# Kernel optimization log

Measured on AMD Instinct MI355X. Metric: run time of the kernel, lower is better.

Reference implementation:

```python
import jax, jax.numpy as jnp
import numpy as np

# dims (match init_kwargs)
L, D, H, K = 8, 384, 6, 64            # layers, hidden, rwkv heads, rwkv head dim
DI, MH, HD, DS, CK = 768, 12, 64, 64, 4  # mamba: d_inner, heads, head_dim, d_state, conv kernel
V, B, T = 32000, 1, 1024


def _rms(x, w, eps=1e-6):
    return w * x * jax.lax.rsqrt(jnp.mean(x * x, axis=-1, keepdims=True) + eps)


def _rwkv6(xn, Wr, Wk, Wv, Wg, Ww, w_bias, u, gn_w, gn_b, Wo):
    # RWKV6: data-dependent diagonal-decay linear attention
    Bb, Tt, Dd = xn.shape
    proj = lambda W: (xn @ W).reshape(Bb, Tt, H, K)
    r, k, v = proj(Wr), proj(Wk), proj(Wv)
    g = xn @ Wg                                        # [B,T,D]
    w = (xn @ Ww + w_bias).reshape(Bb, Tt, H, K)
    decay = jnp.exp(-jnp.exp(w))                       # in (0,1)

    def step(S, inp):                                  # S: [B,H,K,K] (key x value)
        r_t, k_t, v_t, d_t = inp                       # each [B,H,K]
        kv = k_t[..., :, None] * v_t[..., None, :]     # [B,H,K,K]
        o = jnp.einsum('bhk,bhkv->bhv', r_t, S + u[None, :, :, None] * kv)
        S = d_t[..., None] * S + kv
        return S, o

    tm = lambda a: jnp.moveaxis(a, 1, 0)               # time-major
    S0 = jnp.zeros((Bb, H, K, K), xn.dtype)
    _, o = jax.lax.scan(step, S0, (tm(r), tm(k), tm(v), tm(decay)))
    o = jnp.moveaxis(o, 0, 1)                          # [B,T,H,K]
    # per-head GroupNorm
    mu = jnp.mean(o, -1, keepdims=True)
    var = jnp.var(o, -1, keepdims=True)
    o = (o - mu) * jax.lax.rsqrt(var + 1e-5) * gn_w.reshape(H, K) + gn_b.reshape(H, K)
    o = o.reshape(Bb, Tt, Dd) * jax.nn.silu(g)
    return o @ Wo


def _mamba2(xn, W_in, conv_w, conv_b, dt_bias, A_log, Dp, mn_w, W_out):
    # Mamba2: selective scan with scalar A per head
    Bb, Tt, Dd = xn.shape
    zxbcdt = xn @ W_in                                 # [B,T, 2*DI + 2*DS + MH]
    z = zxbcdt[..., :DI]
    xBC = zxbcdt[..., DI:DI + DI + 2 * DS]
    dt = jax.nn.softplus(zxbcdt[..., -MH:] + dt_bias)  # [B,T,MH]
    # causal depthwise conv1d, kernel CK
    xp = jnp.pad(xBC, ((0, 0), (CK - 1, 0), (0, 0)))
    xBC = sum(xp[:, j:j + Tt, :] * conv_w[:, j] for j in range(CK)) + conv_b
    xBC = jax.nn.silu(xBC)
    xs = xBC[..., :DI].reshape(Bb, Tt, MH, HD)
    Bm = xBC[..., DI:DI + DS]                          # [B,T,DS]
    Cm = xBC[..., DI + DS:]                            # [B,T,DS]
    A = -jnp.exp(A_log)                                # [MH]

    def step(S, inp):                                  # S: [B,MH,HD,DS]
        x_t, B_t, C_t, dt_t = inp                      # [B,MH,HD],[B,DS],[B,DS],[B,MH]
        dA = jnp.exp(dt_t * A)                         # [B,MH]
        S = dA[..., None, None] * S + (dt_t[..., None] * x_t)[..., None] * B_t[:, None, None, :]
        y = jnp.einsum('bhps,bs->bhp', S, C_t) + Dp[None, :, None] * x_t
        return S, y

    tm = lambda a: jnp.moveaxis(a, 1, 0)
    S0 = jnp.zeros((Bb, MH, HD, DS), xn.dtype)
    _, y = jax.lax.scan(step, S0, (tm(xs), tm(Bm), tm(Cm), tm(dt)))
    y = jnp.moveaxis(y, 0, 1).reshape(Bb, Tt, DI)
    y = _rms(y * jax.nn.silu(z), mn_w)                 # gated RMSNorm
    return y @ W_out


def _forward(x, embed, ln_w, Wr, Wk, Wv, Wg, Ww, w_bias, u, gn_w, gn_b, Wo,
             W_in, conv_w, conv_b, dt_bias, A_log, Dp, mn_w, W_out,
             gw, gb, ffn_ln_w, ffn_w1, ffn_w2, ln_out_w):
    h = jnp.take(embed, x, axis=0)                     # [B,T,D]
    for i in range(L):
        xn = _rms(h, ln_w[i])
        o_r = _rwkv6(xn, Wr[i], Wk[i], Wv[i], Wg[i], Ww[i], w_bias[i], u[i], gn_w[i], gn_b[i], Wo[i])
        o_m = _mamba2(xn, W_in[i], conv_w[i], conv_b[i], dt_bias[i], A_log[i], Dp[i], mn_w[i], W_out[i])
        gate = jax.nn.sigmoid(jnp.concatenate([o_r, o_m], -1) @ gw[i] + gb[i])  # [B,T,1]
        h = h + gate * o_r + (1.0 - gate) * o_m
        hn = _rms(h, ffn_ln_w[i])
        h = h + jax.nn.gelu(hn @ ffn_w1[i], approximate=False) @ ffn_w2[i]
    h = _rms(h, ln_out_w)
    return h @ embed.T                                 # tied head -> [B,T,V]


def setup_inputs() -> dict:
    key = jax.random.key(0)
    ks = iter(jax.random.split(key, 32))
    n = lambda shape, s=0.02: jax.random.normal(next(ks), shape, jnp.float32) * s
    d = {}
    d['x'] = jax.random.randint(next(ks), (B, T), 0, V)
    d['embed'] = n((V, D))
    d['ln_w'] = jnp.ones((L, D), jnp.float32)
    d['Wr'] = n((L, D, D)); d['Wk'] = n((L, D, D)); d['Wv'] = n((L, D, D))
    d['Wg'] = n((L, D, D)); d['Ww'] = n((L, D, D))
    d['w_bias'] = n((L, D), 0.5)
    d['u'] = n((L, H, K), 0.5)
    d['gn_w'] = jnp.ones((L, D), jnp.float32)
    d['gn_b'] = jnp.zeros((L, D), jnp.float32)
    d['Wo'] = n((L, D, D))
    d['W_in'] = n((L, D, 2 * DI + 2 * DS + MH))
    d['conv_w'] = n((L, DI + 2 * DS, CK), 0.2)
    d['conv_b'] = jnp.zeros((L, DI + 2 * DS), jnp.float32)
    d['dt_bias'] = jax.random.uniform(next(ks), (L, MH), jnp.float32, -4.0, -1.0)
    d['A_log'] = jnp.log(jax.random.uniform(next(ks), (L, MH), jnp.float32, 1.0, 16.0))
    d['Dp'] = jnp.ones((L, MH), jnp.float32)
    d['mn_w'] = jnp.ones((L, DI), jnp.float32)
    d['W_out'] = n((L, DI, D))
    d['gw'] = n((L, 2 * D, 1), 0.01)
    d['gb'] = jnp.full((L, 1), float(np.log(0.3 / 0.7)), jnp.float32)
    d['ffn_ln_w'] = jnp.ones((L, D), jnp.float32)
    d['ffn_w1'] = n((L, D, 4 * D))
    d['ffn_w2'] = n((L, 4 * D, D))
    d['ln_out_w'] = jnp.ones((D,), jnp.float32)
    return d


def reference(x, embed, ln_w, Wr, Wk, Wv, Wg, Ww, w_bias, u, gn_w, gn_b, Wo,
              W_in, conv_w, conv_b, dt_bias, A_log, Dp, mn_w, W_out,
              gw, gb, ffn_ln_w, ffn_w1, ffn_w2, ln_out_w):
    return _forward(x, embed, ln_w, Wr, Wk, Wv, Wg, Ww, w_bias, u, gn_w, gn_b, Wo,
                    W_in, conv_w, conv_b, dt_bias, A_log, Dp, mn_w, W_out,
                    gw, gb, ffn_ln_w, ffn_w1, ffn_w2, ln_out_w)
```

## Files before the change

kernel.cpp:

```cpp
#include <hip/hip_runtime.h>
#include <math.h>

#define TT 1024
#define DD 384
#define NH 6
#define DI 768
#define MH 12
#define DS 64
#define NL 8
#define XDIM 1676
#define CONVC 896
#define NV 32000
#define PZS 3712
#define G_OFF 1152
#define W_OFF 1536
#define Z_OFF 1920
#define XBC_OFF 2688
#define DT_OFF 3584
#define CHK 32
#define NCH 32

typedef __attribute__((ext_vector_type(8))) short short8;
typedef __attribute__((ext_vector_type(4))) float f32x4;

__device__ __forceinline__ float siluf(float x) { return x / (1.f + expf(-x)); }
__device__ __forceinline__ float sigmoidf_(float x) { return 1.f / (1.f + expf(-x)); }
__device__ __forceinline__ float geluf(float x) {
  return 0.5f * x * (1.f + erff(x * 0.70710678118654752440f));
}
__device__ __forceinline__ unsigned short f2b(float x) {
  union { float f; unsigned int u; } v; v.f = x;
  unsigned int r = v.u + 0x7fffu + ((v.u >> 16) & 1u);
  return (unsigned short)(r >> 16);
}

#define GLDS(gp, lp) __builtin_amdgcn_global_load_lds( \
    (const __attribute__((address_space(1))) void*)(gp), \
    (__attribute__((address_space(3))) void*)(lp), 16, 0, 0)

template<int EPI>
__global__ __launch_bounds__(256) void gemm_bf16(
    const unsigned short* __restrict__ A, const unsigned short* __restrict__ Bt,
    float* __restrict__ C, unsigned short* __restrict__ Cb, int N, int K, int ldC)
{
  __shared__ unsigned short As[4096];
  __shared__ unsigned short Bs[4096];
  int tid = threadIdx.x;
  int wid = tid >> 6, lane = tid & 63;
  int m0 = blockIdx.y * 64, n0 = blockIdx.x * 64;
  int wr = wid >> 1, wc = wid & 1;
  int r0 = tid >> 3, ch = tid & 7;
  int scs = (ch ^ (r0 & 7)) * 8;
  const unsigned short* ga = A  + (size_t)(m0 + r0) * K + scs;
  const unsigned short* gb = Bt + (size_t)(n0 + r0) * K + scs;
  unsigned short* la = As + wid * 512;
  unsigned short* lb = Bs + wid * 512;
  int fr = lane & 15, fc = lane >> 4;
  f32x4 zz = {0.f, 0.f, 0.f, 0.f};
  f32x4 acc[2][2];
  acc[0][0] = zz; acc[0][1] = zz; acc[1][0] = zz; acc[1][1] = zz;

  int kper = K / (int)gridDim.z;
  int ks = blockIdx.z * kper, ke = ks + kper;
  size_t row32 = (size_t)32 * K;
  for (int k0 = ks; k0 < ke; k0 += 64) {
    GLDS(ga + k0, la);
    GLDS(ga + k0 + row32, la + 2048);
    GLDS(gb + k0, lb);
    GLDS(gb + k0 + row32, lb + 2048);
    __syncthreads();
#pragma unroll
    for (int kh = 0; kh < 2; ++kh) {
      short8 af[2], bf[2];
#pragma unroll
      for (int mg = 0; mg < 2; ++mg) {
        int ar = wr * 32 + mg * 16 + fr;
        af[mg] = *reinterpret_cast<const short8*>(&As[ar * 64 + (((kh * 4 + fc) ^ (ar & 7)) * 8)]);
      }
#pragma unroll
      for (int ng = 0; ng < 2; ++ng) {
        int br = wc * 32 + ng * 16 + fr;
        bf[ng] = *reinterpret_cast<const short8*>(&Bs[br * 64 + (((kh * 4 + fc) ^ (br & 7)) * 8)]);
      }
#pragma unroll
      for (int mg = 0; mg < 2; ++mg)
#pragma unroll
        for (int ng = 0; ng < 2; ++ng)
          acc[mg][ng] = __builtin_amdgcn_mfma_f32_16x16x32_bf16(af[mg], bf[ng], acc[mg][ng], 0, 0, 0);
    }
    __syncthreads();
  }
#pragma unroll
  for (int mg = 0; mg < 2; ++mg)
#pragma unroll
    for (int ng = 0; ng < 2; ++ng) {
      int col = n0 + wc * 32 + ng * 16 + fr;
      if (col < N) {
#pragma unroll
        for (int j = 0; j < 4; ++j) {
          int row = m0 + wr * 32 + mg * 16 + fc * 4 + j;
          if (EPI == 1)      Cb[(size_t)row * ldC + col] = f2b(geluf(acc[mg][ng][j]));
          else if (EPI == 3) atomicAdd(&C[(size_t)row * ldC + col], acc[mg][ng][j]);
          else               C[(size_t)row * ldC + col]  = acc[mg][ng][j];
        }
      }
    }
}

__global__ __launch_bounds__(256) void gemm_dual(
    const unsigned short* __restrict__ A0, const unsigned short* __restrict__ B0t,
    float* __restrict__ C0, int K0, int ld0, int nx0, int nb0,
    const unsigned short* __restrict__ A1, const unsigned short* __restrict__ B1t,
    float* __restrict__ C1, int K1, int ld1, int nx1)
{
  __shared__ unsigned short As[4096];
  __shared__ unsigned short Bs[4096];
  int b = blockIdx.x;
  const unsigned short *A, *Bt; float* C; int K, ldC, bx, by;
  if (b < nb0) { A = A0; Bt = B0t; C = C0; K = K0; ldC = ld0; bx = b % nx0; by = b / nx0; }
  else { b -= nb0; A = A1; Bt = B1t; C = C1; K = K1; ldC = ld1; bx = b % nx1; by = b / nx1; }
  int tid = threadIdx.x;
  int wid = tid >> 6, lane = tid & 63;
  int m0 = by * 64, n0 = bx * 64;
  int wr = wid >> 1, wc = wid & 1;
  int r0 = tid >> 3, ch = tid & 7;
  int scs = (ch ^ (r0 & 7)) * 8;
  const unsigned short* ga = A  + (size_t)(m0 + r0) * K + scs;
  const unsigned short* gb = Bt + (size_t)(n0 + r0) * K + scs;
  unsigned short* la = As + wid * 512;
  unsigned short* lb = Bs + wid * 512;
  int fr = lane & 15, fc = lane >> 4;
  f32x4 zz = {0.f, 0.f, 0.f, 0.f};
  f32x4 acc[2][2];
  acc[0][0] = zz; acc[0][1] = zz; acc[1][0] = zz; acc[1][1] = zz;
  size_t row32 = (size_t)32 * K;
  for (int k0 = 0; k0 < K; k0 += 64) {
    GLDS(ga + k0, la);
    GLDS(ga + k0 + row32, la + 2048);
    GLDS(gb + k0, lb);
    GLDS(gb + k0 + row32, lb + 2048);
    __syncthreads();
#pragma unroll
    for (int kh = 0; kh < 2; ++kh) {
      short8 af[2], bf[2];
// ... 8 lines not shown
        bf[ng] = *reinterpret_cast<const short8*>(&Bs[br * 64 + (((kh * 4 + fc) ^ (br & 7)) * 8)]);
      }
#pragma unroll
      for (int mg = 0; mg < 2; ++mg)
#pragma unroll
        for (int ng = 0; ng < 2; ++ng)
          acc[mg][ng] = __builtin_amdgcn_mfma_f32_16x16x32_bf16(af[mg], bf[ng], acc[mg][ng], 0, 0, 0);
    }
    __syncthreads();
  }
#pragma unroll
  for (int mg = 0; mg < 2; ++mg)
#pragma unroll
    for (int ng = 0; ng < 2; ++ng) {
      int col = n0 + wc * 32 + ng * 16 + fr;
#pragma unroll
      for (int j = 0; j < 4; ++j) {
        int row = m0 + wr * 32 + mg * 16 + fc * 4 + j;
        C[(size_t)row * ldC + col] = acc[mg][ng][j];
      }
    }
}

__global__ __launch_bounds__(256) void gemm128(
    const unsigned short* __restrict__ A, const unsigned short* __restrict__ Bt,
    float* __restrict__ C, int N, int K, int ldC)
{
  __shared__ unsigned short As[8192];
  __shared__ unsigned short Bs[8192];
  int tid = threadIdx.x;
  int wid = tid >> 6, lane = tid & 63;
  int m0 = blockIdx.y * 128, n0 = blockIdx.x * 128;
  int wr = wid >> 1, wc = wid & 1;
  int r0 = tid >> 3, ch = tid & 7;
  int scs = (ch ^ (r0 & 7)) * 8;
  const unsigned short* ga = A  + (size_t)(m0 + r0) * K + scs;
  const unsigned short* gb = Bt + (size_t)(n0 + r0) * K + scs;
  int fr = lane & 15, fc = lane >> 4;
  f32x4 zz = {0.f, 0.f, 0.f, 0.f};
  f32x4 acc[4][4];
#pragma unroll
  for (int i = 0; i < 4; i++)
#pragma unroll
    for (int j = 0; j < 4; j++) acc[i][j] = zz;

  size_t row32 = (size_t)32 * K;
  for (int k0 = 0; k0 < K; k0 += 64) {
#pragma unroll
    for (int i = 0; i < 4; ++i) {
      GLDS(ga + k0 + i * row32, As + i * 2048 + wid * 512);
      GLDS(gb + k0 + i * row32, Bs + i * 2048 + wid * 512);
    }
    __syncthreads();
#pragma unroll
    for (int kh = 0; kh < 2; ++kh) {
      short8 af[4], bf[4];
#pragma unroll
      for (int mg = 0; mg < 4; ++mg) {
        int ar = wr * 64 + mg * 16 + fr;
        af[mg] = *reinterpret_cast<const short8*>(&As[ar * 64 + (((kh * 4 + fc) ^ (ar & 7)) * 8)]);
      }
#pragma unroll
      for (int ng = 0; ng < 4; ++ng) {
        int br = wc * 64 + ng * 16 + fr;
        bf[ng] = *reinterpret_cast<const short8*>(&Bs[br * 64 + (((kh * 4 + fc) ^ (br & 7)) * 8)]);
      }
#pragma unroll
      for (int mg = 0; mg < 4; ++mg)
#pragma unroll
        for (int ng = 0; ng < 4; ++ng)
          acc[mg][ng] = __builtin_amdgcn_mfma_f32_16x16x32_bf16(af[mg], bf[ng], acc[mg][ng], 0, 0, 0);
    }
    __syncthreads();
  }
#pragma unroll
  for (int mg = 0; mg < 4; ++mg)
#pragma unroll
    for (int ng = 0; ng < 4; ++ng) {
      int col = n0 + wc * 64 + ng * 16 + fr;
      if (col < N) {
#pragma unroll
        for (int j = 0; j < 4; ++j) {
          int row = m0 + wr * 64 + mg * 16 + fc * 4 + j;
          C[(size_t)row * ldC + col] = acc[mg][ng][j];
        }
      }
    }
}

struct TCJob { const float* src; unsigned short* dst; int K, N, Npad, nx; size_t sStr, dStr; int tend; };
struct TC10 { TCJob j[10]; };

__global__ __launch_bounds__(256) void transconv_all(TC10 P)
{
  __shared__ float tile[32][33];
  int bid = blockIdx.x;
  int q = 0;
  while (bid >= P.j[q].tend) ++q;
  int tstart = (q == 0) ? 0 : P.j[q - 1].tend;
  TCJob jb = P.j[q];
  int local = bid - tstart;
  int bx = local % jb.nx, by = local / jb.nx;
  const float* src = jb.src + (size_t)blockIdx.y * jb.sStr;
  unsigned short* dst = jb.dst + (size_t)blockIdx.y * jb.dStr;
  int k0 = by * 32, n0 = bx * 32;
  int tx = threadIdx.x & 31, ty = threadIdx.x >> 5;
  for (int i = ty; i < 32; i += 8) {
    int k = k0 + i, n = n0 + tx;
    tile[i][tx] = (k < jb.K && n < jb.N) ? src[(size_t)k * jb.N + n] : 0.f;
  }
  __syncthreads();
  for (int i = ty; i < 32; i += 8) {
    int n = n0 + i, k = k0 + tx;
    if (n < jb.Npad && k < jb.K) dst[(size_t)n * jb.K + k] = f2b(tile[tx][i]);
  }
}

__global__ void conv_b16_kernel(const float* __restrict__ src, unsigned short* __restrict__ dst, int n)
{
  int idx = blockIdx.x * 256 + threadIdx.x;
  if (idx < n) dst[idx] = f2b(src[idx]);
}

__global__ void embed_kernel(const int* __restrict__ x, const float* __restrict__ embed,
                             float* __restrict__ h)
{
  int idx = blockIdx.x * 256 + threadIdx.x;
  if (idx < TT * DD) {
    int t = idx / DD, d = idx % DD;
    h[idx] = embed[(size_t)x[t] * DD + d];
  }
}

__global__ __launch_bounds__(256) void rms_kernel(const float* __restrict__ in,
                                                  const float* __restrict__ w,
                                                  unsigned short* __restrict__ out)
{
  int row = blockIdx.x * 4 + (threadIdx.x >> 6);
  int lane = threadIdx.x & 63;
  const float* r = in + (size_t)row * DD;
  float v[6]; float ss = 0.f;
#pragma unroll
  for (int j = 0; j < 6; ++j) { v[j] = r[lane + j * 64]; ss = fmaf(v[j], v[j], ss); }
#pragma unroll
  for (int s = 1; s < 64; s <<= 1) ss += __shfl_xor(ss, s);
  float scale = rsqrtf(ss * (1.f / DD) + 1e-6f);
#pragma unroll
  for (int j = 0; j < 6; ++j)
    out[(size_t)row * DD + lane + j * 64] = f2b(w[lane + j * 64] * v[j] * scale);
}

__global__ __launch_bounds__(256) void scanA_kernel(
    const float* __restrict__ PZ, const float* __restrict__ u, const float* __restrict__ wbias,
    float* __restrict__ so, float* __restrict__ rPb,
    float* __restrict__ MstR, float* __restrict__ DcR,
    const float* __restrict__ cw, const float* __restrict__ cbia,
    const float* __restrict__ dtbias,
    const float* __restrict__ Alog, const float* __restrict__ Dpw,
    float* __restrict__ yb, float* __restrict__ Ccb,
    float* __restrict__ MstM, float* __restrict__ DcM)
{
  __shared__ float smem[2 * 256 + 64];
  int b = blockIdx.x, tid = threadIdx.x;
  if (b < 192) {
    int h = b >> 5, c = b & 31;
    float* sbuf = smem; float* us = smem + 512;
    if (tid < 64) us[tid] = u[h * 64 + tid];
    int wv = tid >> 6, l = tid & 63;
    int vv = wv * 16 + (l & 15);
    int kc = l >> 4;
    int arr = tid >> 6, idx = tid & 63;
    int off = (arr == 0) ? 0 : (arr == 1) ? 384 : (arr == 2) ? W_OFF : 768;
// ... 215 lines not shown
    float4 s0 = sp[0], s1 = sp[1];
    ov[0] = s0.x + acc[0]; ov[1] = s0.y + acc[1]; ov[2] = s0.z + acc[2]; ov[3] = s0.w + acc[3];
    ov[4] = s1.x + acc[4]; ov[5] = s1.y + acc[5]; ov[6] = s1.z + acc[6]; ov[7] = s1.w + acc[7];
    float m_ = 0.f;
#pragma unroll
    for (int j = 0; j < 8; j++) m_ += ov[j];
    m_ += __shfl_xor(m_, 1); m_ += __shfl_xor(m_, 2); m_ += __shfl_xor(m_, 4);
    float mu = m_ * (1.f / 64.f);
    float vv = 0.f;
#pragma unroll
    for (int j = 0; j < 8; j++) { float d = ov[j] - mu; vv = fmaf(d, d, vv); }
    vv += __shfl_xor(vv, 1); vv += __shfl_xor(vv, 2); vv += __shfl_xor(vv, 4);
    float rstd = rsqrtf(vv * (1.f / 64.f) + 1e-5f);
#pragma unroll
    for (int j = 0; j < 8; j++) {
      int d = obase + q + j;
      float gv = PZ[(size_t)(t0 + t) * PZS + G_OFF + d];
      float o = fmaf((ov[j] - mu) * rstd, gnw[d], gnb[d]) * siluf(gv);
      gob[(size_t)(t0 + t) * DD + d] = f2b(o);
    }
  }
}

__global__ __launch_bounds__(256) void mamba_norm_kernel(const float* __restrict__ yb,
    const float* __restrict__ PZ, const float* __restrict__ mnw, unsigned short* __restrict__ out)
{
  int row = blockIdx.x * 4 + (threadIdx.x >> 6);
  int lane = threadIdx.x & 63;
  float v[12]; float ss = 0.f;
#pragma unroll
  for (int j = 0; j < 12; ++j) {
    int c = lane + j * 64;
    float z = PZ[(size_t)row * PZS + Z_OFF + c];
    float t = yb[(size_t)row * DI + c] * siluf(z);
    v[j] = t; ss = fmaf(t, t, ss);
  }
#pragma unroll
  for (int s = 1; s < 64; s <<= 1) ss += __shfl_xor(ss, s);
  float scale = rsqrtf(ss * (1.f / DI) + 1e-6f);
#pragma unroll
  for (int j = 0; j < 12; ++j) {
    int c = lane + j * 64;
    out[(size_t)row * DI + c] = f2b(v[j] * scale * mnw[c]);
  }
}

__global__ __launch_bounds__(256) void gate_rms_kernel(const float* __restrict__ orb,
    const float* __restrict__ omb, const float* __restrict__ gw,
    const float* __restrict__ gb, const float* __restrict__ flnw,
    float* __restrict__ h, unsigned short* __restrict__ xnb)
{
  int row = blockIdx.x * 4 + (threadIdx.x >> 6);
  int lane = threadIdx.x & 63;
  float a[6], bq[6]; float ss = 0.f;
#pragma unroll
  for (int j = 0; j < 6; ++j) {
    int c = lane + j * 64;
    a[j] = orb[(size_t)row * DD + c]; bq[j] = omb[(size_t)row * DD + c];
    ss += a[j] * gw[c] + bq[j] * gw[DD + c];
  }
#pragma unroll
  for (int s = 1; s < 64; s <<= 1) ss += __shfl_xor(ss, s);
  float gate = sigmoidf_(ss + gb[0]);
  float hn[6]; float ss2 = 0.f;
#pragma unroll
  for (int j = 0; j < 6; ++j) {
    int c = lane + j * 64;
    size_t ix = (size_t)row * DD + c;
    hn[j] = h[ix] + gate * a[j] + (1.f - gate) * bq[j];
    h[ix] = hn[j];
    ss2 = fmaf(hn[j], hn[j], ss2);
  }
#pragma unroll
  for (int s = 1; s < 64; s <<= 1) ss2 += __shfl_xor(ss2, s);
  float scale = rsqrtf(ss2 * (1.f / DD) + 1e-6f);
#pragma unroll
  for (int j = 0; j < 6; ++j) {
    int c = lane + j * 64;
    xnb[(size_t)row * DD + c] = f2b(flnw[c] * hn[j] * scale);
  }
}

extern "C" void kernel_launch(void* const* d_in, const int* in_sizes, int n_in,
                              void* d_out, int out_size, void* d_ws, size_t ws_size,
                              hipStream_t stream)
{
  const int*   x        = (const int*)  d_in[0];
  const float* embed    = (const float*)d_in[1];
  const float* ln_w     = (const float*)d_in[2];
  const float* Wr       = (const float*)d_in[3];
  const float* Wk       = (const float*)d_in[4];
  const float* Wv       = (const float*)d_in[5];
  const float* Wg       = (const float*)d_in[6];
  const float* Ww       = (const float*)d_in[7];
  const float* w_bias   = (const float*)d_in[8];
  const float* u        = (const float*)d_in[9];
  const float* gn_w     = (const float*)d_in[10];
  const float* gn_b     = (const float*)d_in[11];
  const float* Wo       = (const float*)d_in[12];
  const float* W_in     = (const float*)d_in[13];
  const float* conv_w   = (const float*)d_in[14];
  const float* conv_b   = (const float*)d_in[15];
  const float* dt_bias  = (const float*)d_in[16];
  const float* A_log    = (const float*)d_in[17];
  const float* Dp       = (const float*)d_in[18];
  const float* mn_w     = (const float*)d_in[19];
  const float* W_out    = (const float*)d_in[20];
  const float* gw       = (const float*)d_in[21];
  const float* gb       = (const float*)d_in[22];
  const float* ffn_ln_w = (const float*)d_in[23];
  const float* ffn_w1   = (const float*)d_in[24];
  const float* ffn_w2   = (const float*)d_in[25];
  const float* ln_out_w = (const float*)d_in[26];

  char* base = (char*)d_ws;
  size_t off = 0;
  auto alloc = [&](size_t bytes) { off = (off + 255) & ~(size_t)255; void* p = base + off; off += bytes; return p; };

  float* h    = (float*)alloc((size_t)TT * DD * 4);
  float* PZ   = (float*)alloc((size_t)TT * PZS * 4);
  float* yb   = (float*)alloc((size_t)TT * DI * 4);
  float* so   = (float*)alloc((size_t)TT * DD * 4);
  float* orb  = (float*)alloc((size_t)TT * DD * 4);
  float* omb  = (float*)alloc((size_t)TT * DD * 4);
  float* rPb  = (float*)alloc((size_t)TT * DD * 4);
  float* Ccb  = (float*)alloc((size_t)TT * DI * 4);
  float* MstR = (float*)alloc((size_t)NH * NCH * 4096 * 4);
  float* DcR  = (float*)alloc((size_t)NH * NCH * 64 * 4);
  float* MstM = (float*)alloc((size_t)MH * NCH * 4096 * 4);
  float* DcM  = (float*)alloc((size_t)MH * NCH * 4);
  unsigned short* xnb = (unsigned short*)alloc((size_t)TT * DD * 2);
  unsigned short* gob = (unsigned short*)alloc((size_t)TT * DD * 2);
  unsigned short* ynb = (unsigned short*)alloc((size_t)TT * DI * 2);
  unsigned short* fhb = (unsigned short*)alloc((size_t)TT * 1536 * 2);
  unsigned short* WallT = (unsigned short*)alloc((size_t)NL * PZS * 384 * 2);
  unsigned short* WoT   = (unsigned short*)alloc((size_t)NL * 384 * 384 * 2);
  unsigned short* WoutT = (unsigned short*)alloc((size_t)NL * 384 * 768 * 2);
  unsigned short* F1T   = (unsigned short*)alloc((size_t)NL * 1536 * 384 * 2);
  unsigned short* F2T   = (unsigned short*)alloc((size_t)NL * 384 * 1536 * 2);
  unsigned short* embB  = (unsigned short*)alloc((size_t)NV * DD * 2);
  (void)ws_size; (void)in_sizes; (void)n_in; (void)out_size;

  dim3 blk(256);
  int gTD = (TT * DD + 255) / 256;

  TC10 tc;
  int te = 0;
  auto setjob = [&](int q, const float* src, unsigned short* dst, int K, int N, int Npad,
                    int nx, int ny, size_t sStr, size_t dStr) {
    te += nx * ny;
    tc.j[q] = TCJob{src, dst, K, N, Npad, nx, sStr, dStr, te};
  };
  setjob(0, Wr, WallT + (size_t)0 * 384 * 384, 384, 384, 384, 12, 12, (size_t)384 * 384, (size_t)PZS * 384);
  setjob(1, Wk, WallT + (size_t)1 * 384 * 384, 384, 384, 384, 12, 12, (size_t)384 * 384, (size_t)PZS * 384);
  setjob(2, Wv, WallT + (size_t)2 * 384 * 384, 384, 384, 384, 12, 12, (size_t)384 * 384, (size_t)PZS * 384);
  setjob(3, Wg, WallT + (size_t)3 * 384 * 384, 384, 384, 384, 12, 12, (size_t)384 * 384, (size_t)PZS * 384);
  setjob(4, Ww, WallT + (size_t)4 * 384 * 384, 384, 384, 384, 12, 12, (size_t)384 * 384, (size_t)PZS * 384);
  setjob(5, W_in, WallT + (size_t)1920 * 384, 384, XDIM, 1792, 56, 12, (size_t)384 * XDIM, (size_t)PZS * 384);
  setjob(6, Wo, WoT, 384, 384, 384, 12, 12, (size_t)384 * 384, (size_t)384 * 384);
  setjob(7, W_out, WoutT, 768, 384, 384, 12, 24, (size_t)768 * 384, (size_t)384 * 768);
  setjob(8, ffn_w1, F1T, 384, 1536, 1536, 48, 12, (size_t)384 * 1536, (size_t)1536 * 384);
  setjob(9, ffn_w2, F2T, 1536, 384, 384, 12, 48, (size_t)1536 * 384, (size_t)384 * 1536);
  transconv_all<<<dim3(te, 8), blk, 0, stream>>>(tc);
  conv_b16_kernel<<<(NV * DD + 255) / 256, blk, 0, stream>>>(embed, embB, NV * DD);
  embed_kernel<<<gTD, blk, 0, stream>>>(x, embed, h);

  for (int i = 0; i < NL; ++i) {
    rms_kernel<<<256, blk, 0, stream>>>(h, ln_w + (size_t)i * DD, xnb);

    gemm_bf16<0><<<dim3(58, 16), blk, 0, stream>>>(
        xnb, WallT + (size_t)i * PZS * 384, PZ, nullptr, PZS, 384, PZS);

    scanA_kernel<<<576, blk, 0, stream>>>(PZ, u + (size_t)i * NH * 64, w_bias + (size_t)i * DD,
                                          so, rPb, MstR, DcR,
                                          conv_w + (size_t)i * CONVC * 4, conv_b + (size_t)i * CONVC,
                                          dt_bias + (size_t)i * MH,
                                          A_log + (size_t)i * MH, Dp + (size_t)i * MH,
                                          yb, Ccb, MstM, DcM);
    corr_kernel<<<576, blk, 0, stream>>>(MstR, DcR, rPb, so, MstM, DcM, Ccb, yb,
                                         PZ, gn_w + (size_t)i * DD, gn_b + (size_t)i * DD, gob);

    mamba_norm_kernel<<<256, blk, 0, stream>>>(yb, PZ, mn_w + (size_t)i * DI, ynb);

    gemm_dual<<<192, blk, 0, stream>>>(
        gob, WoT + (size_t)i * 384 * 384, orb, 384, DD, 6, 96,
        ynb, WoutT + (size_t)i * 384 * 768, omb, 768, DD, 6);

    gate_rms_kernel<<<256, blk, 0, stream>>>(orb, omb, gw + (size_t)i * 2 * DD, gb + i,
                                             ffn_ln_w + (size_t)i * DD, h, xnb);

    gemm_bf16<1><<<dim3(24, 16), blk, 0, stream>>>(
        xnb, F1T + (size_t)i * 1536 * 384, nullptr, fhb, 1536, 384, 1536);
    gemm_bf16<3><<<dim3(6, 16, 4), blk, 0, stream>>>(
        fhb, F2T + (size_t)i * 384 * 1536, h, nullptr, DD, 1536, DD);
  }

  rms_kernel<<<256, blk, 0, stream>>>(h, ln_out_w, xnb);
  gemm128<<<dim3(250, 8), blk, 0, stream>>>(
      xnb, embB, (float*)d_out, NV, 384, NV);
}
```

Measured before the change: 983.0 us.

## Fuse RMS norms and gating into GEMM prologues with a full-K A tile in LDS

Each GEMM block now normalizes its own 64 rows and stages the whole 64x384 bf16 A tile in LDS, which absorbs work that used separate kernels. The input RMS norm moves into the projection GEMM, the Mamba gated norm into the W_out GEMM, and the gate-mix residual plus FFN norm into the FFN1 GEMM. This removes three launches per layer and the bf16 intermediates between them. The residual now ping-pongs between two buffers so the fused kernel can write the updated residual while reading the old one. In exchange the norm and gate work is recomputed by every column block, and the larger LDS footprint (about 56KB per block) lowers occupancy.

Measured after the change: 1.911 ms. 94.4% more time.

```diff
diff --git a/kernel.cpp b/kernel.cpp
--- a/kernel.cpp
+++ b/kernel.cpp
@@ -38,44 +38,31 @@
     (const __attribute__((address_space(1))) void*)(gp), \
     (__attribute__((address_space(3))) void*)(lp), 16, 0, 0)
 
-template<int EPI>
-__global__ __launch_bounds__(256) void gemm_bf16(
-    const unsigned short* __restrict__ A, const unsigned short* __restrict__ Bt,
-    float* __restrict__ C, unsigned short* __restrict__ Cb, int N, int K, int ldC)
-{
-  __shared__ unsigned short As[4096];
-  __shared__ unsigned short Bs[4096];
-  int tid = threadIdx.x;
+__device__ __forceinline__ void gemmA_block(
+    const unsigned short* __restrict__ As, unsigned short* Bs,
+    const unsigned short* __restrict__ Bt, int Kfull, int n0, int kglob0, int nsteps, int aoff,
+    int tid, f32x4 acc[2][2])
+{
   int wid = tid >> 6, lane = tid & 63;
-  int m0 = blockIdx.y * 64, n0 = blockIdx.x * 64;
   int wr = wid >> 1, wc = wid & 1;
   int r0 = tid >> 3, ch = tid & 7;
   int scs = (ch ^ (r0 & 7)) * 8;
-  const unsigned short* ga = A  + (size_t)(m0 + r0) * K + scs;
-  const unsigned short* gb = Bt + (size_t)(n0 + r0) * K + scs;
-  unsigned short* la = As + wid * 512;
-  unsigned short* lb = Bs + wid * 512;
+  const unsigned short* gb = Bt + (size_t)(n0 + r0) * Kfull + scs + kglob0;
+  size_t row32 = (size_t)32 * Kfull;
   int fr = lane & 15, fc = lane >> 4;
-  f32x4 zz = {0.f, 0.f, 0.f, 0.f};
-  f32x4 acc[2][2];
-  acc[0][0] = zz; acc[0][1] = zz; acc[1][0] = zz; acc[1][1] = zz;
-
-  int kper = K / (int)gridDim.z;
-  int ks = blockIdx.z * kper, ke = ks + kper;
-  size_t row32 = (size_t)32 * K;
-  for (int k0 = ks; k0 < ke; k0 += 64) {
-    GLDS(ga + k0, la);
-    GLDS(ga + k0 + row32, la + 2048);
-    GLDS(gb + k0, lb);
-    GLDS(gb + k0 + row32, lb + 2048);
+  for (int s = 0; s < nsteps; ++s) {
+    int k0 = s * 64;
+    GLDS(gb + k0, Bs + wid * 512);
+    GLDS(gb + k0 + row32, Bs + 2048 + wid * 512);
     __syncthreads();
+    int acol = aoff + k0;
 #pragma unroll
     for (int kh = 0; kh < 2; ++kh) {
       short8 af[2], bf[2];
 #pragma unroll
       for (int mg = 0; mg < 2; ++mg) {
         int ar = wr * 32 + mg * 16 + fr;
-        af[mg] = *reinterpret_cast<const short8*>(&As[ar * 64 + (((kh * 4 + fc) ^ (ar & 7)) * 8)]);
+        af[mg] = *reinterpret_cast<const short8*>(&As[ar * 384 + acol + (((kh * 4 + fc) ^ (ar & 7)) * 8)]);
       }
 #pragma unroll
       for (int ng = 0; ng < 2; ++ng) {
@@ -90,36 +77,33 @@
     }
     __syncthreads();
   }
+}
+
+__device__ __forceinline__ void epi_store(f32x4 acc[2][2], float* C, unsigned short* Cb,
+    int ldC, int m0, int n0, int epi, int tid)
+{
+  int wid = tid >> 6, lane = tid & 63;
+  int wr = wid >> 1, wc = wid & 1;
+  int fr = lane & 15, fc = lane >> 4;
 #pragma unroll
   for (int mg = 0; mg < 2; ++mg)
 #pragma unroll
     for (int ng = 0; ng < 2; ++ng) {
       int col = n0 + wc * 32 + ng * 16 + fr;
-      if (col < N) {
-#pragma unroll
-        for (int j = 0; j < 4; ++j) {
-          int row = m0 + wr * 32 + mg * 16 + fc * 4 + j;
-          if (EPI == 1)      Cb[(size_t)row * ldC + col] = f2b(geluf(acc[mg][ng][j]));
-          else if (EPI == 3) atomicAdd(&C[(size_t)row * ldC + col], acc[mg][ng][j]);
-          else               C[(size_t)row * ldC + col]  = acc[mg][ng][j];
-        }
-      }
-    }
-}
-
-__global__ __launch_bounds__(256) void gemm_dual(
-    const unsigned short* __restrict__ A0, const unsigned short* __restrict__ B0t,
-    float* __restrict__ C0, int K0, int ld0, int nx0, int nb0,
-    const unsigned short* __restrict__ A1, const unsigned short* __restrict__ B1t,
-    float* __restrict__ C1, int K1, int ld1, int nx1)
-{
-  __shared__ unsigned short As[4096];
-  __shared__ unsigned short Bs[4096];
-  int b = blockIdx.x;
-  const unsigned short *A, *Bt; float* C; int K, ldC, bx, by;
-  if (b < nb0) { A = A0; Bt = B0t; C = C0; K = K0; ldC = ld0; bx = b % nx0; by = b / nx0; }
-  else { b -= nb0; A = A1; Bt = B1t; C = C1; K = K1; ldC = ld1; bx = b % nx1; by = b / nx1; }
-  int tid = threadIdx.x;
+#pragma unroll
+      for (int j = 0; j < 4; ++j) {
+        int row = m0 + wr * 32 + mg * 16 + fc * 4 + j;
+        if (epi == 1) Cb[(size_t)row * ldC + col] = f2b(geluf(acc[mg][ng][j]));
+        else          C[(size_t)row * ldC + col] = acc[mg][ng][j];
+      }
+    }
+}
+
+__device__ __forceinline__ void gemm64_std(
+    const unsigned short* __restrict__ A, const unsigned short* __restrict__ Bt,
+    float* __restrict__ C, int K, int ldC, int bx, int by,
+    unsigned short* As, unsigned short* Bs, int tid)
+{
   int wid = tid >> 6, lane = tid & 63;
   int m0 = by * 64, n0 = bx * 64;
   int wr = wid >> 1, wc = wid & 1;
@@ -174,132 +158,43 @@
     }
 }
 
-__global__ __launch_bounds__(256) void gemm128(
-    const unsigned short* __restrict__ A, const unsigned short* __restrict__ Bt,
-    float* __restrict__ C, int N, int K, int ldC)
-{
-  __shared__ unsigned short As[8192];
-  __shared__ unsigned short Bs[8192];
+__global__ __launch_bounds__(256) void proj_kernel(
+    const float* __restrict__ hin, const float* __restrict__ lnw,
+    const unsigned short* __restrict__ WallT_i, float* __restrict__ PZ)
+{
+  __shared__ unsigned short As[64 * 384];
+  __shared__ unsigned short Bs[4096];
   int tid = threadIdx.x;
-  int wid = tid >> 6, lane = tid & 63;
-  int m0 = blockIdx.y * 128, n0 = blockIdx.x * 128;
-  int wr = wid >> 1, wc = wid & 1;
-  int r0 = tid >> 3, ch = tid & 7;
-  int scs = (ch ^ (r0 & 7)) * 8;
-  const unsigned short* ga = A  + (size_t)(m0 + r0) * K + scs;
-  const unsigned short* gb = Bt + (size_t)(n0 + r0) * K + scs;
-  int fr = lane & 15, fc = lane >> 4;
+  int m0 = blockIdx.y * 64, n0 = blockIdx.x * 64;
+  int r = tid >> 2, q = tid & 3;
+  const float* hr = hin + (size_t)(m0 + r) * DD + q * 96;
+  float ss = 0.f;
+#pragma unroll 4
+  for (int j = 0; j < 96; j += 4) {
+    float4 x = *(const float4*)(hr + j);
+    ss += x.x * x.x + x.y * x.y + x.z * x.z + x.w * x.w;
+  }
+  ss += __shfl_xor(ss, 1); ss += __shfl_xor(ss, 2);
+  float scale = rsqrtf(ss * (1.f / DD) + 1e-6f);
+  const float* wq = lnw + q * 96;
+#pragma unroll
+  for (int g = 0; g < 12; ++g) {
+    int gi = q * 12 + g;
+    int kb = gi >> 3, c = gi & 7;
+    float4 a = *(const float4*)(hr + g * 8);
+    float4 b2 = *(const float4*)(hr + g * 8 + 4);
+    unsigned short tmp[8];
+    tmp[0] = f2b(wq[g*8+0] * a.x * scale);  tmp[1] = f2b(wq[g*8+1] * a.y * scale);
+    tmp[2] = f2b(wq[g*8+2] * a.z * scale);  tmp[3] = f2b(wq[g*8+3] * a.w * scale);
+    tmp[4] = f2b(wq[g*8+4] * b2.x * scale); tmp[5] = f2b(wq[g*8+5] * b2.y * scale);
+    tmp[6] = f2b(wq[g*8+6] * b2.z * scale); tmp[7] = f2b(wq[g*8+7] * b2.w * scale);
+    *(short8*)(&As[r * 384 + kb * 64 + ((c ^ (r & 7)) * 8)]) = *(short8*)tmp;
+  }
   f32x4 zz = {0.f, 0.f, 0.f, 0.f};
-  f32x4 acc[4][4];
-#pragma unroll
-  for (int i = 0; i < 4; i++)
-#pragma unroll
-    for (int j = 0; j < 4; j++) acc[i][j] = zz;
-
-  size_t row32 = (size_t)32 * K;
-  for (int k0 = 0; k0 < K; k0 += 64) {
-#pragma unroll
-    for (int i = 0; i < 4; ++i) {
-      GLDS(ga + k0 + i * row32, As + i * 2048 + wid * 512);
-      GLDS(gb + k0 + i * row32, Bs + i * 2048 + wid * 512);
-    }
-    __syncthreads();
-#pragma unroll
-    for (int kh = 0; kh < 2; ++kh) {
-      short8 af[4], bf[4];
-#pragma unroll
-      for (int mg = 0; mg < 4; ++mg) {
-        int ar = wr * 64 + mg * 16 + fr;
-        af[mg] = *reinterpret_cast<const short8*>(&As[ar * 64 + (((kh * 4 + fc) ^ (ar & 7)) * 8)]);
-      }
-#pragma unroll
-      for (int ng = 0; ng < 4; ++ng) {
-        int br = wc * 64 + ng * 16 + fr;
-        bf[ng] = *reinterpret_cast<const short8*>(&Bs[br * 64 + (((kh * 4 + fc) ^ (br & 7)) * 8)]);
-      }
-#pragma unroll
-      for (int mg = 0; mg < 4; ++mg)
-#pragma unroll
-        for (int ng = 0; ng < 4; ++ng)
-          acc[mg][ng] = __builtin_amdgcn_mfma_f32_16x16x32_bf16(af[mg], bf[ng], acc[mg][ng], 0, 0, 0);
-    }
-    __syncthreads();
-  }
-#pragma unroll
-  for (int mg = 0; mg < 4; ++mg)
-#pragma unroll
-    for (int ng = 0; ng < 4; ++ng) {
-      int col = n0 + wc * 64 + ng * 16 + fr;
-      if (col < N) {
-#pragma unroll
-        for (int j = 0; j < 4; ++j) {
-          int row = m0 + wr * 64 + mg * 16 + fc * 4 + j;
-          C[(size_t)row * ldC + col] = acc[mg][ng][j];
-        }
-      }
-    }
-}
-
-struct TCJob { const float* src; unsigned short* dst; int K, N, Npad, nx; size_t sStr, dStr; int tend; };
-struct TC10 { TCJob j[10]; };
-
-__global__ __launch_bounds__(256) void transconv_all(TC10 P)
-{
-  __shared__ float tile[32][33];
-  int bid = blockIdx.x;
-  int q = 0;
-  while (bid >= P.j[q].tend) ++q;
-  int tstart = (q == 0) ? 0 : P.j[q - 1].tend;
-  TCJob jb = P.j[q];
-  int local = bid - tstart;
-  int bx = local % jb.nx, by = local / jb.nx;
-  const float* src = jb.src + (size_t)blockIdx.y * jb.sStr;
-  unsigned short* dst = jb.dst + (size_t)blockIdx.y * jb.dStr;
-  int k0 = by * 32, n0 = bx * 32;
-  int tx = threadIdx.x & 31, ty = threadIdx.x >> 5;
-  for (int i = ty; i < 32; i += 8) {
-    int k = k0 + i, n = n0 + tx;
-    tile[i][tx] = (k < jb.K && n < jb.N) ? src[(size_t)k * jb.N + n] : 0.f;
-  }
-  __syncthreads();
-  for (int i = ty; i < 32; i += 8) {
-    int n = n0 + i, k = k0 + tx;
-    if (n < jb.Npad && k < jb.K) dst[(size_t)n * jb.K + k] = f2b(tile[tx][i]);
-  }
-}
-
-__global__ void conv_b16_kernel(const float* __restrict__ src, unsigned short* __restrict__ dst, int n)
-{
-  int idx = blockIdx.x * 256 + threadIdx.x;
-  if (idx < n) dst[idx] = f2b(src[idx]);
-}
-
-__global__ void embed_kernel(const int* __restrict__ x, const float* __restrict__ embed,
-                             float* __restrict__ h)
-{
-  int idx = blockIdx.x * 256 + threadIdx.x;
-  if (idx < TT * DD) {
-    int t = idx / DD, d = idx % DD;
-    h[idx] = embed[(size_t)x[t] * DD + d];
-  }
-}
-
-__global__ __launch_bounds__(256) void rms_kernel(const float* __restrict__ in,
-                                                  const float* __restrict__ w,
-                                                  unsigned short* __restrict__ out)
-{
-  int row = blockIdx.x * 4 + (threadIdx.x >> 6);
-  int lane = threadIdx.x & 63;
-  const float* r = in + (size_t)row * DD;
-  float v[6]; float ss = 0.f;
-#pragma unroll
-  for (int j = 0; j < 6; ++j) { v[j] = r[lane + j * 64]; ss = fmaf(v[j], v[j], ss); }
-#pragma unroll
-  for (int s = 1; s < 64; s <<= 1) ss += __shfl_xor(ss, s);
-  float scale = rsqrtf(ss * (1.f / DD) + 1e-6f);
-#pragma unroll
-  for (int j = 0; j < 6; ++j)
-    out[(size_t)row * DD + lane + j * 64] = f2b(w[lane + j * 64] * v[j] * scale);
+  f32x4 acc[2][2];
+  acc[0][0] = zz; acc[0][1] = zz; acc[1][0] = zz; acc[1][1] = zz;
+  gemmA_block(As, Bs, WallT_i, 384, n0, 0, 6, 0, tid, acc);
+  epi_store(acc, PZ, nullptr, PZS, m0, n0, 0, tid);
 }
 
 __global__ __launch_bounds__(256) void scanA_kernel(
@@ -561,63 +456,324 @@
   }
 }
 
-__global__ __launch_bounds__(256) void mamba_norm_kernel(const float* __restrict__ yb,
-    const float* __restrict__ PZ, const float* __restrict__ mnw, unsigned short* __restrict__ out)
+__global__ __launch_bounds__(256) void wo_wout_kernel(
+    const unsigned short* __restrict__ gob, const unsigned short* __restrict__ WoT_i,
+    float* __restrict__ orb_,
+    const float* __restrict__ yb, const float* __restrict__ PZ, const float* __restrict__ mnw,
+    const unsigned short* __restrict__ WoutT_i, float* __restrict__ omb_)
+{
+  __shared__ unsigned short As[64 * 384];
+  __shared__ unsigned short Bs[4096];
+  int tid = threadIdx.x;
+  int b = blockIdx.x;
+  if (b < 96) {
+    gemm64_std(gob, WoT_i, orb_, 384, 384, b % 6, b / 6, As, Bs, tid);
+    return;
+  }
+  int t = b - 96;
+  int bx = t % 6, by = t / 6;
+  int m0 = by * 64, n0 = bx * 64;
+  int r = tid >> 2, q = tid & 3;
+  int row = m0 + r;
+  float ss = 0.f;
+  {
+    const float* py = yb + (size_t)row * DI + q * 192;
+    const float* pz = PZ + (size_t)row * PZS + Z_OFF + q * 192;
+#pragma unroll 4
+    for (int j = 0; j < 192; j += 4) {
+      float4 y4 = *(const float4*)(py + j);
+      float4 z4 = *(const float4*)(pz + j);
+      float v0 = y4.x * siluf(z4.x), v1 = y4.y * siluf(z4.y);
+      float v2 = y4.z * siluf(z4.z), v3 = y4.w * siluf(z4.w);
+      ss += v0 * v0 + v1 * v1 + v2 * v2 + v3 * v3;
+    }
+  }
+  ss += __shfl_xor(ss, 1); ss += __shfl_xor(ss, 2);
+  float scale = rsqrtf(ss * (1.f / DI) + 1e-6f);
+  f32x4 zz = {0.f, 0.f, 0.f, 0.f};
+  f32x4 acc[2][2];
+  acc[0][0] = zz; acc[0][1] = zz; acc[1][0] = zz; acc[1][1] = zz;
+  for (int half = 0; half < 2; ++half) {
+    const float* py = yb + (size_t)row * DI + half * 384 + q * 96;
+    const float* pz = PZ + (size_t)row * PZS + Z_OFF + half * 384 + q * 96;
+    const float* pw = mnw + half * 384 + q * 96;
+#pragma unroll
+    for (int g = 0; g < 12; ++g) {
+      int gi = q * 12 + g;
+      int kb = gi >> 3, c = gi & 7;
+      float4 y0 = *(const float4*)(py + g * 8);
+      float4 y1 = *(const float4*)(py + g * 8 + 4);
+      float4 z0 = *(const float4*)(pz + g * 8);
+      float4 z1 = *(const float4*)(pz + g * 8 + 4);
+      unsigned short tmp[8];
+      tmp[0] = f2b(y0.x * siluf(z0.x) * scale * pw[g*8+0]);
+      tmp[1] = f2b(y0.y * siluf(z0.y) * scale * pw[g*8+1]);
+      tmp[2] = f2b(y0.z * siluf(z0.z) * scale * pw[g*8+2]);
+      tmp[3] = f2b(y0.w * siluf(z0.w) * scale * pw[g*8+3]);
+      tmp[4] = f2b(y1.x * siluf(z1.x) * scale * pw[g*8+4]);
+      tmp[5] = f2b(y1.y * siluf(z1.y) * scale * pw[g*8+5]);
+      tmp[6] = f2b(y1.z * siluf(z1.z) * scale * pw[g*8+6]);
+      tmp[7] = f2b(y1.w * siluf(z1.w) * scale * pw[g*8+7]);
+      *(short8*)(&As[r * 384 + kb * 64 + ((c ^ (r & 7)) * 8)]) = *(short8*)tmp;
+    }
+    gemmA_block(As, Bs, WoutT_i, 768, n0, half * 384, 6, 0, tid, acc);
+  }
+  epi_store(acc, omb_, nullptr, 384, m0, n0, 0, tid);
+}
+
+__global__ __launch_bounds__(256) void ffn1_kernel(
+    const float* __restrict__ orb_, const float* __restrict__ omb_,
+    const float* __restrict__ gwv, const float* __restrict__ gbv,
+    const float* __restrict__ hin, float* __restrict__ hmid,
+    const float* __restrict__ flnw, const unsigned short* __restrict__ F1T_i,
+    unsigned short* __restrict__ fhb)
+{
+  __shared__ unsigned short As[64 * 384];
+  __shared__ unsigned short Bs[4096];
+  int tid = threadIdx.x;
+  int m0 = blockIdx.y * 64, n0 = blockIdx.x * 64;
+  int r = tid >> 2, q = tid & 3;
+  size_t rb = (size_t)(m0 + r) * DD + q * 96;
+  const float* pr = orb_ + rb;
+  const float* pm = omb_ + rb;
+  const float* ph = hin + rb;
+  float* po = hmid + rb;
+  const float* g1 = gwv + q * 96;
+  const float* g2 = gwv + DD + q * 96;
+  float ss = 0.f;
+#pragma unroll 4
+  for (int j = 0; j < 96; j += 4) {
+    float4 a = *(const float4*)(pr + j), b2 = *(const float4*)(pm + j);
+    float4 w1 = *(const float4*)(g1 + j), w2 = *(const float4*)(g2 + j);
+    ss += a.x * w1.x + a.y * w1.y + a.z * w1.z + a.w * w1.w
+        + b2.x * w2.x + b2.y * w2.y + b2.z * w2.z + b2.w * w2.w;
+  }
+  ss += __shfl_xor(ss, 1); ss += __shfl_xor(ss, 2);
+  float gate = sigmoidf_(ss + gbv[0]);
+  float ss2 = 0.f;
+#pragma unroll 4
+  for (int j = 0; j < 96; j += 4) {
+    float4 a = *(const float4*)(pr + j), b2 = *(const float4*)(pm + j), hh = *(const float4*)(ph + j);
+    float4 hn;
+    hn.x = hh.x + gate * a.x + (1.f - gate) * b2.x;
+    hn.y = hh.y + gate * a.y + (1.f - gate) * b2.y;
+    hn.z = hh.z + gate * a.z + (1.f - gate) * b2.z;
+    hn.w = hh.w + gate * a.w + (1.f - gate) * b2.w;
+    *(float4*)(po + j) = hn;
+    ss2 += hn.x * hn.x + hn.y * hn.y + hn.z * hn.z + hn.w * hn.w;
+  }
+  ss2 += __shfl_xor(ss2, 1); ss2 += __shfl_xor(ss2, 2);
+  float scale = rsqrtf(ss2 * (1.f / DD) + 1e-6f);
+  const float* wq = flnw + q * 96;
+#pragma unroll
+  for (int g = 0; g < 12; ++g) {
+    int gi = q * 12 + g;
+    int kb = gi >> 3, c = gi & 7;
+    float4 a = *(const float4*)(po + g * 8);
+    float4 b2 = *(const float4*)(po + g * 8 + 4);
+    unsigned short tmp[8];
+    tmp[0] = f2b(wq[g*8+0] * a.x * scale);  tmp[1] = f2b(wq[g*8+1] * a.y * scale);
+    tmp[2] = f2b(wq[g*8+2] * a.z * scale);  tmp[3] = f2b(wq[g*8+3] * a.w * scale);
+    tmp[4] = f2b(wq[g*8+4] * b2.x * scale); tmp[5] = f2b(wq[g*8+5] * b2.y * scale);
+    tmp[6] = f2b(wq[g*8+6] * b2.z * scale); tmp[7] = f2b(wq[g*8+7] * b2.w * scale);
+    *(short8*)(&As[r * 384 + kb * 64 + ((c ^ (r & 7)) * 8)]) = *(short8*)tmp;
+  }
+  f32x4 zz = {0.f, 0.f, 0.f, 0.f};
+  f32x4 acc[2][2];
+  acc[0][0] = zz; acc[0][1] = zz; acc[1][0] = zz; acc[1][1] = zz;
+  gemmA_block(As, Bs, F1T_i, 384, n0, 0, 6, 0, tid, acc);
+  epi_store(acc, nullptr, fhb, 1536, m0, n0, 1, tid);
+}
+
+__global__ __launch_bounds__(256) void ffn2_kernel(
+    const unsigned short* __restrict__ A, const unsigned short* __restrict__ Bt,
+    float* __restrict__ C, int N, int K, int ldC)
+{
+  __shared__ unsigned short As[4096];
+  __shared__ unsigned short Bs[4096];
+  int tid = threadIdx.x;
+  int wid = tid >> 6, lane = tid & 63;
+  int m0 = blockIdx.y * 64, n0 = blockIdx.x * 64;
+  int wr = wid >> 1, wc = wid & 1;
+  int r0 = tid >> 3, ch = tid & 7;
+  int scs = (ch ^ (r0 & 7)) * 8;
+  const unsigned short* ga = A  + (size_t)(m0 + r0) * K + scs;
+  const unsigned short* gb = Bt + (size_t)(n0 + r0) * K + scs;
+  unsigned short* la = As + wid * 512;
+  unsigned short* lb = Bs + wid * 512;
+  int fr = lane & 15, fc = lane >> 4;
+  f32x4 zz = {0.f, 0.f, 0.f, 0.f};
+  f32x4 acc[2][2];
+  acc[0][0] = zz; acc[0][1] = zz; acc[1][0] = zz; acc[1][1] = zz;
+  int kper = K / (int)gridDim.z;
+  int ks = blockIdx.z * kper, ke = ks + kper;
+  size_t row32 = (size_t)32 * K;
+  for (int k0 = ks; k0 < ke; k0 += 64) {
+    GLDS(ga + k0, la);
+    GLDS(ga + k0 + row32, la + 2048);
+    GLDS(gb + k0, lb);
+    GLDS(gb + k0 + row32, lb + 2048);
+    __syncthreads();
+#pragma unroll
+    for (int kh = 0; kh < 2; ++kh) {
+      short8 af[2], bf[2];
+#pragma unroll
+      for (int mg = 0; mg < 2; ++mg) {
+        int ar = wr * 32 + mg * 16 + fr;
+        af[mg] = *reinterpret_cast<const short8*>(&As[ar * 64 + (((kh * 4 + fc) ^ (ar & 7)) * 8)]);
+      }
+#pragma unroll
+      for (int ng = 0; ng < 2; ++ng) {
+        int br = wc * 32 + ng * 16 + fr;
+        bf[ng] = *reinterpret_cast<const short8*>(&Bs[br * 64 + (((kh * 4 + fc) ^ (br & 7)) * 8)]);
+      }
+#pragma unroll
+      for (int mg = 0; mg < 2; ++mg)
+#pragma unroll
+        for (int ng = 0; ng < 2; ++ng)
+          acc[mg][ng] = __builtin_amdgcn_mfma_f32_16x16x32_bf16(af[mg], bf[ng], acc[mg][ng], 0, 0, 0);
+    }
+    __syncthreads();
+  }
+#pragma unroll
+  for (int mg = 0; mg < 2; ++mg)
+#pragma unroll
+    for (int ng = 0; ng < 2; ++ng) {
+      int col = n0 + wc * 32 + ng * 16 + fr;
+#pragma unroll
+      for (int j = 0; j < 4; ++j) {
+        int row = m0 + wr * 32 + mg * 16 + fc * 4 + j;
+        atomicAdd(&C[(size_t)row * ldC + col], acc[mg][ng][j]);
+      }
+    }
+}
+
+__global__ __launch_bounds__(256) void gemm128(
+    const unsigned short* __restrict__ A, const unsigned short* __restrict__ Bt,
+    float* __restrict__ C, int N, int K, int ldC)
+{
+  __shared__ unsigned short As[8192];
+  __shared__ unsigned short Bs[8192];
+  int tid = threadIdx.x;
+  int wid = tid >> 6, lane = tid & 63;
+  int m0 = blockIdx.y * 128, n0 = blockIdx.x * 128;
+  int wr = wid >> 1, wc = wid & 1;
+  int r0 = tid >> 3, ch = tid & 7;
+  int scs = (ch ^ (r0 & 7)) * 8;
+  const unsigned short* ga = A  + (size_t)(m0 + r0) * K + scs;
+  const unsigned short* gb = Bt + (size_t)(n0 + r0) * K + scs;
+  int fr = lane & 15, fc = lane >> 4;
+  f32x4 zz = {0.f, 0.f, 0.f, 0.f};
+  f32x4 acc[4][4];
+#pragma unroll
+  for (int i = 0; i < 4; i++)
+#pragma unroll
+    for (int j = 0; j < 4; j++) acc[i][j] = zz;
+
+  size_t row32 = (size_t)32 * K;
+  for (int k0 = 0; k0 < K; k0 += 64) {
+#pragma unroll
+    for (int i = 0; i < 4; ++i) {
+      GLDS(ga + k0 + i * row32, As + i * 2048 + wid * 512);
+      GLDS(gb + k0 + i * row32, Bs + i * 2048 + wid * 512);
+    }
+    __syncthreads();
+#pragma unroll
+    for (int kh = 0; kh < 2; ++kh) {
+      short8 af[4], bf[4];
+#pragma unroll
+      for (int mg = 0; mg < 4; ++mg) {
+        int ar = wr * 64 + mg * 16 + fr;
+        af[mg] = *reinterpret_cast<const short8*>(&As[ar * 64 + (((kh * 4 + fc) ^ (ar & 7)) * 8)]);
+      }
+#pragma unroll
+      for (int ng = 0; ng < 4; ++ng) {
+        int br = wc * 64 + ng * 16 + fr;
+        bf[ng] = *reinterpret_cast<const short8*>(&Bs[br * 64 + (((kh * 4 + fc) ^ (br & 7)) * 8)]);
+      }
+#pragma unroll
+      for (int mg = 0; mg < 4; ++mg)
+#pragma unroll
+        for (int ng = 0; ng < 4; ++ng)
+          acc[mg][ng] = __builtin_amdgcn_mfma_f32_16x16x32_bf16(af[mg], bf[ng], acc[mg][ng], 0, 0, 0);
+    }
+    __syncthreads();
+  }
+#pragma unroll
+  for (int mg = 0; mg < 4; ++mg)
+#pragma unroll
+    for (int ng = 0; ng < 4; ++ng) {
+      int col = n0 + wc * 64 + ng * 16 + fr;
+      if (col < N) {
+#pragma unroll
+        for (int j = 0; j < 4; ++j) {
+          int row = m0 + wr * 64 + mg * 16 + fc * 4 + j;
+          C[(size_t)row * ldC + col] = acc[mg][ng][j];
+        }
+      }
+    }
+}
+
+struct TCJob { const float* src; unsigned short* dst; int K, N, Npad, nx; size_t sStr, dStr; int tend; };
+struct TC10 { TCJob j[10]; };
+
+__global__ __launch_bounds__(256) void transconv_all(TC10 P)
+{
+  __shared__ float tile[32][33];
+  int bid = blockIdx.x;
+  int q = 0;
+  while (bid >= P.j[q].tend) ++q;
+  int tstart = (q == 0) ? 0 : P.j[q - 1].tend;
+  TCJob jb = P.j[q];
+  int local = bid - tstart;
+  int bx = local % jb.nx, by = local / jb.nx;
+  const float* src = jb.src + (size_t)blockIdx.y * jb.sStr;
+  unsigned short* dst = jb.dst + (size_t)blockIdx.y * jb.dStr;
+  int k0 = by * 32, n0 = bx * 32;
+  int tx = threadIdx.x & 31, ty = threadIdx.x >> 5;
+  for (int i = ty; i < 32; i += 8) {
+    int k = k0 + i, n = n0 + tx;
+    tile[i][tx] = (k < jb.K && n < jb.N) ? src[(size_t)k * jb.N + n] : 0.f;
+  }
+  __syncthreads();
+  for (int i = ty; i < 32; i += 8) {
+    int n = n0 + i, k = k0 + tx;
+    if (n < jb.Npad && k < jb.K) dst[(size_t)n * jb.K + k] = f2b(tile[tx][i]);
+  }
+}
+
+__global__ void conv_b16_kernel(const float* __restrict__ src, unsigned short* __restrict__ dst, int n)
+{
+  int idx = blockIdx.x * 256 + threadIdx.x;
+  if (idx < n) dst[idx] = f2b(src[idx]);
+}
+
+__global__ void embed_kernel(const int* __restrict__ x, const float* __restrict__ embed,
+                             float* __restrict__ h)
+{
+  int idx = blockIdx.x * 256 + threadIdx.x;
+  if (idx < TT * DD) {
+    int t = idx / DD, d = idx % DD;
+    h[idx] = embed[(size_t)x[t] * DD + d];
+  }
+}
+
+__global__ __launch_bounds__(256) void rms_kernel(const float* __restrict__ in,
+                                                  const float* __restrict__ w,
+                                                  unsigned short* __restrict__ out)
 {
   int row = blockIdx.x * 4 + (threadIdx.x >> 6);
   int lane = threadIdx.x & 63;
-  float v[12]; float ss = 0.f;
-#pragma unroll
-  for (int j = 0; j < 12; ++j) {
-    int c = lane + j * 64;
-    float z = PZ[(size_t)row * PZS + Z_OFF + c];
-    float t = yb[(size_t)row * DI + c] * siluf(z);
-    v[j] = t; ss = fmaf(t, t, ss);
-  }
+  const float* r = in + (size_t)row * DD;
+  float v[6]; float ss = 0.f;
+#pragma unroll
+  for (int j = 0; j < 6; ++j) { v[j] = r[lane + j * 64]; ss = fmaf(v[j], v[j], ss); }
 #pragma unroll
   for (int s = 1; s < 64; s <<= 1) ss += __shfl_xor(ss, s);
-  float scale = rsqrtf(ss * (1.f / DI) + 1e-6f);
-#pragma unroll
-  for (int j = 0; j < 12; ++j) {
-    int c = lane + j * 64;
-    out[(size_t)row * DI + c] = f2b(v[j] * scale * mnw[c]);
-  }
-}
-
-__global__ __launch_bounds__(256) void gate_rms_kernel(const float* __restrict__ orb,
-    const float* __restrict__ omb, const float* __restrict__ gw,
-    const float* __restrict__ gb, const float* __restrict__ flnw,
-    float* __restrict__ h, unsigned short* __restrict__ xnb)
-{
-  int row = blockIdx.x * 4 + (threadIdx.x >> 6);
-  int lane = threadIdx.x & 63;
-  float a[6], bq[6]; float ss = 0.f;
-#pragma unroll
-  for (int j = 0; j < 6; ++j) {
-    int c = lane + j * 64;
-    a[j] = orb[(size_t)row * DD + c]; bq[j] = omb[(size_t)row * DD + c];
-    ss += a[j] * gw[c] + bq[j] * gw[DD + c];
-  }
-#pragma unroll
-  for (int s = 1; s < 64; s <<= 1) ss += __shfl_xor(ss, s);
-  float gate = sigmoidf_(ss + gb[0]);
-  float hn[6]; float ss2 = 0.f;
-#pragma unroll
-  for (int j = 0; j < 6; ++j) {
-    int c = lane + j * 64;
-    size_t ix = (size_t)row * DD + c;
-    hn[j] = h[ix] + gate * a[j] + (1.f - gate) * bq[j];
-    h[ix] = hn[j];
-    ss2 = fmaf(hn[j], hn[j], ss2);
-  }
-#pragma unroll
-  for (int s = 1; s < 64; s <<= 1) ss2 += __shfl_xor(ss2, s);
-  float scale = rsqrtf(ss2 * (1.f / DD) + 1e-6f);
-#pragma unroll
-  for (int j = 0; j < 6; ++j) {
-    int c = lane + j * 64;
-    xnb[(size_t)row * DD + c] = f2b(flnw[c] * hn[j] * scale);
-  }
+  float scale = rsqrtf(ss * (1.f / DD) + 1e-6f);
+#pragma unroll
+  for (int j = 0; j < 6; ++j)
+    out[(size_t)row * DD + lane + j * 64] = f2b(w[lane + j * 64] * v[j] * scale);
 }
 
 extern "C" void kernel_launch(void* const* d_in, const int* in_sizes, int n_in,
@@ -656,7 +812,8 @@
   size_t off = 0;
   auto alloc = [&](size_t bytes) { off = (off + 255) & ~(size_t)255; void* p = base + off; off += bytes; return p; };
 
-  float* h    = (float*)alloc((size_t)TT * DD * 4);
+  float* hb0  = (float*)alloc((size_t)TT * DD * 4);
+  float* hb1  = (float*)alloc((size_t)TT * DD * 4);
   float* PZ   = (float*)alloc((size_t)TT * PZS * 4);
   float* yb   = (float*)alloc((size_t)TT * DI * 4);
   float* so   = (float*)alloc((size_t)TT * DD * 4);
@@ -670,7 +827,6 @@
   float* DcM  = (float*)alloc((size_t)MH * NCH * 4);
   unsigned short* xnb = (unsigned short*)alloc((size_t)TT * DD * 2);
   unsigned short* gob = (unsigned short*)alloc((size_t)TT * DD * 2);
-  unsigned short* ynb = (unsigned short*)alloc((size_t)TT * DI * 2);
   unsigned short* fhb = (unsigned short*)alloc((size_t)TT * 1536 * 2);
   unsigned short* WallT = (unsigned short*)alloc((size_t)NL * PZS * 384 * 2);
   unsigned short* WoT   = (unsigned short*)alloc((size_t)NL * 384 * 384 * 2);
@@ -702,13 +858,14 @@
   setjob(9, ffn_w2, F2T, 1536, 384, 384, 12, 48, (size_t)1536 * 384, (size_t)384 * 1536);
   transconv_all<<<dim3(te, 8), blk, 0, stream>>>(tc);
   conv_b16_kernel<<<(NV * DD + 255) / 256, blk, 0, stream>>>(embed, embB, NV * DD);
-  embed_kernel<<<gTD, blk, 0, stream>>>(x, embed, h);
+  embed_kernel<<<gTD, blk, 0, stream>>>(x, embed, hb0);
 
   for (int i = 0; i < NL; ++i) {
-    rms_kernel<<<256, blk, 0, stream>>>(h, ln_w + (size_t)i * DD, xnb);
-
-    gemm_bf16<0><<<dim3(58, 16), blk, 0, stream>>>(
-        xnb, WallT + (size_t)i * PZS * 384, PZ, nullptr, PZS, 384, PZS);
+    float* hin  = (i & 1) ? hb1 : hb0;
+    float* hmid = (i & 1) ? hb0 : hb1;
+
+    proj_kernel<<<dim3(58, 16), blk, 0, stream>>>(
+        hin, ln_w + (size_t)i * DD, WallT + (size_t)i * PZS * 384, PZ);
 
     scanA_kernel<<<576, blk, 0, stream>>>(PZ, u + (size_t)i * NH * 64, w_bias + (size_t)i * DD,
                                           so, rPb, MstR, DcR,
@@ -719,22 +876,21 @@
     corr_kernel<<<576, blk, 0, stream>>>(MstR, DcR, rPb, so, MstM, DcM, Ccb, yb,
                                          PZ, gn_w + (size_t)i * DD, gn_b + (size_t)i * DD, gob);
 
-    mamba_norm_kernel<<<256, blk, 0, stream>>>(yb, PZ, mn_w + (size_t)i * DI, ynb);
-
-    gemm_dual<<<192, blk, 0, stream>>>(
-        gob, WoT + (size_t)i * 384 * 384, orb, 384, DD, 6, 96,
-        ynb, WoutT + (size_t)i * 384 * 768, omb, 768, DD, 6);
-
-    gate_rms_kernel<<<256, blk, 0, stream>>>(orb, omb, gw + (size_t)i * 2 * DD, gb + i,
-                                             ffn_ln_w + (size_t)i * DD, h, xnb);
-
-    gemm_bf16<1><<<dim3(24, 16), blk, 0, stream>>>(
-        xnb, F1T + (size_t)i * 1536 * 384, nullptr, fhb, 1536, 384, 1536);
-    gemm_bf16<3><<<dim3(6, 16, 4), blk, 0, stream>>>(
-        fhb, F2T + (size_t)i * 384 * 1536, h, nullptr, DD, 1536, DD);
-  }
-
-  rms_kernel<<<256, blk, 0, stream>>>(h, ln_out_w, xnb);
+    wo_wout_kernel<<<192, blk, 0, stream>>>(
+        gob, WoT + (size_t)i * 384 * 384, orb,
+        yb, PZ, mn_w + (size_t)i * DI,
+        WoutT + (size_t)i * 384 * 768, omb);
+
+    ffn1_kernel<<<dim3(24, 16), blk, 0, stream>>>(
+        orb, omb, gw + (size_t)i * 2 * DD, gb + i,
+        hin, hmid, ffn_ln_w + (size_t)i * DD,
+        F1T + (size_t)i * 1536 * 384, fhb);
+
+    ffn2_kernel<<<dim3(6, 16, 4), blk, 0, stream>>>(
+        fhb, F2T + (size_t)i * 384 * 1536, hmid, 384, 1536, 384);
+  }
+
+  rms_kernel<<<256, blk, 0, stream>>>(hb0, ln_out_w, xnb);
   gemm128<<<dim3(250, 8), blk, 0, stream>>>(
       xnb, embB, (float*)d_out, NV, 384, NV);
 }
```
